# Kernel optimization log

Hardware: AMD Instinct MI355X
Metric: run time of the kernel (lower is better)

Reference implementation:

```python
import jax, jax.numpy as jnp
import numpy as np

B, S, D = 4, 4096, 2048
DH = D // 2
EPS = 1e-6


def setup_inputs() -> dict:
    key = jax.random.key(0)
    ks = jax.random.split(key, 6)
    return {
        "inputs": jax.random.normal(ks[0], (B * S, D), jnp.float32),
        "lf1_cache": jax.random.normal(ks[1], (B, D, 1, 1), jnp.float32),
        "lf2_cache": jax.random.normal(ks[2], (B, DH, 1, 1), jnp.float32),
        "w1": jax.random.normal(ks[3], (DH, D, 2), jnp.float32) / np.sqrt(2.0 * D).astype(np.float32),
        "b1": jnp.zeros((DH,), jnp.float32),
        "w2": jax.random.normal(ks[4], (D, DH, 2), jnp.float32) / np.sqrt(2.0 * DH).astype(np.float32),
        "b2": jnp.zeros((D,), jnp.float32),
        "ln_w": jnp.ones((D,), jnp.float32),
    }


def reference(inputs, lf1_cache, lf2_cache, w1, b1, w2, b2, ln_w):
    # inputs: [B*S, D] flat tokens; caches hold one previous timestep per batch.
    x = inputs.reshape(B, S, D)
    # prepend cached timestep -> [B, S+1, D]  (equiv. to torch.cat along conv time dim)
    x_cat = jnp.concatenate([lf1_cache[:, :, 0, 0][:, None, :], x], axis=1)
    # conv1: kernel size 2 over time, dense over channels (groups=1)
    # o1[b,t,e] = sum_d w1[e,d,0]*x_cat[b,t,d] + w1[e,d,1]*x_cat[b,t+1,d] + b1[e]
    o1 = (jnp.einsum('btd,ed->bte', x_cat[:, :-1], w1[:, :, 0])
          + jnp.einsum('btd,ed->bte', x_cat[:, 1:], w1[:, :, 1]) + b1)  # [B,S,DH]
    o1_cat = jnp.concatenate([lf2_cache[:, :, 0, 0][:, None, :], o1], axis=1)  # [B,S+1,DH]
    o2 = (jnp.einsum('bte,de->btd', o1_cat[:, :-1], w2[:, :, 0])
          + jnp.einsum('bte,de->btd', o1_cat[:, 1:], w2[:, :, 1]) + b2)  # [B,S,D]
    y = o2 + x  # residual add
    # RMSNorm over the channel dim
    inv_rms = jax.lax.rsqrt(jnp.mean(y * y, axis=-1, keepdims=True) + EPS)
    lf_output = y * inv_rms * ln_w  # [B, S, D]
    # new caches: last timestep of conv1 input and conv2 input, in [B,C,1,1] layout
    lf1 = x_cat[:, -1][:, :, None, None]
    lf2 = o1_cat[:, -1][:, :, None, None]
    return lf_output, lf1, lf2
```

## Files before the change

### kernel.cpp

```cpp
#include <hip/hip_runtime.h>
#include <cstdint>

#define BB 4
#define SS 4096
#define DD 2048
#define DH 1024
#define MM (BB * SS)
#define EPSV 1e-6f

typedef unsigned short u16;
typedef __bf16 bf16x8 __attribute__((ext_vector_type(8)));
typedef float f32x4 __attribute__((ext_vector_type(4)));


__device__ __forceinline__ u16 f2bf(float f) {
    uint32_t u = __float_as_uint(f);
    u += 0x7fffu + ((u >> 16) & 1u);
    return (u16)(u >> 16);
}

__device__ __forceinline__ void async16(const void* g, void* l) {
    __builtin_amdgcn_global_load_lds(
        (const __attribute__((address_space(1))) uint32_t*)g,
        (__attribute__((address_space(3))) uint32_t*)l,
        16, 0, 0);
}

#define FENCE asm volatile("" ::: "memory")


__global__ void cvt_f32_bf16(const float* __restrict__ in, u16* __restrict__ out, long n4) {
    long i = (long)blockIdx.x * blockDim.x + threadIdx.x;
    if (i >= n4) return;
    float4 v = *(const float4*)(in + i * 4);
    ushort4 o;
    o.x = f2bf(v.x); o.y = f2bf(v.y); o.z = f2bf(v.z); o.w = f2bf(v.w);
    *(ushort4*)(out + i * 4) = o;
}

__global__ void pack_w(const float* __restrict__ in, u16* __restrict__ out, int dshift) {
    int idx = blockIdx.x * 256 + threadIdx.x;
    int Dd = 1 << dshift;
    int e = idx >> dshift;
    int d = idx & (Dd - 1);
    float2 v = *(const float2*)(in + (long)idx * 2);
    long rowbase = (long)e * (Dd * 2);
    out[rowbase + d] = f2bf(v.x);
    out[rowbase + Dd + d] = f2bf(v.y);
}

template <int KD, int MODE>
__launch_bounds__(512, 2)
__global__ void gemm2tap(const u16* __restrict__ A,
                         const u16* __restrict__ cache,
                         const u16* __restrict__ Bt,
                         const float* __restrict__ bias,
                         u16* __restrict__ obf,
                         float* __restrict__ lf2out,
                         const float* __restrict__ xres,
                         float* __restrict__ yout)
{
    constexpr int KTOT = 2 * KD;
    constexpr int NT = KTOT / 64;
    constexpr int NS = 2 * NT;
    constexpr int NN = (MODE == 1) ? DH : DD;
    static_assert(NS % 4 == 0 && NS >= 8, "ring-4 schedule needs NS % 4 == 0, NS >= 8");

    const int tid = threadIdx.x;
    const int lane = tid & 63;
    const int wave = tid >> 6;
    const int bm = blockIdx.x;
    const int bn = blockIdx.y;

    __shared__ __align__(16) u16 sm[65536];

    const int srow = wave * 16 + (lane >> 2);
    const int skc  = (lane & 3) ^ ((lane >> 3) & 3);
    const int sRowA = wave * 512;

    const u16 *aPrev0, *aPrev1, *aCur0, *aCur1, *bPtr0, *bPtr1;
    {
        long r0 = (long)bm * 256 + srow;
        long r1 = r0 + 128;
        aCur0 = A + r0 * KD + skc * 8;
        aCur1 = A + r1 * KD + skc * 8;
        aPrev0 = ((((int)r0) & (SS - 1)) == 0) ? (cache + (r0 >> 12) * KD + skc * 8)
                                               : (A + (r0 - 1) * KD + skc * 8);
        aPrev1 = ((((int)r1) & (SS - 1)) == 0) ? (cache + (r1 >> 12) * KD + skc * 8)
                                               : (A + (r1 - 1) * KD + skc * 8);
        long n0l = (long)bn * 256 + srow;
        bPtr0 = Bt + n0l * KTOT + skc * 8;
        bPtr1 = Bt + (n0l + 128) * KTOT + skc * 8;
    }

#define STAGE(SLOT_, U_) do {                                                  \
        const int _u = (U_);                                                   \
        const u16 *_g0, *_g1;                                                  \
        if (_u < NT) { _g0 = aPrev0 + _u * 32; _g1 = aPrev1 + _u * 32; }       \
        else { _g0 = aCur0 + (_u - NT) * 32; _g1 = aCur1 + (_u - NT) * 32; }   \
        async16(_g0, sm + (SLOT_) * 8192 + sRowA);                             \
        async16(_g1, sm + (SLOT_) * 8192 + 4096 + sRowA);                      \
        async16(bPtr0 + _u * 32, sm + 32768 + (SLOT_) * 8192 + sRowA);         \
        async16(bPtr1 + _u * 32, sm + 32768 + (SLOT_) * 8192 + 4096 + sRowA);  \
    } while (0)

    const int frow = lane & 15;
    const int fquad = lane >> 4;
    const int wm128 = (wave >> 2) * 128;
    const int wn64  = (wave & 3) * 64;
    const int fq8s = (fquad ^ ((frow >> 1) & 3)) * 8;
    const int afb = (wm128 + frow) * 32 + fq8s;
    const int bfb = (wn64 + frow) * 32 + fq8s;

    f32x4 acc[8][4];
#pragma unroll
    for (int i = 0; i < 8; ++i)
#pragma unroll
        for (int j = 0; j < 4; ++j)
            acc[i][j] = (f32x4){0.f, 0.f, 0.f, 0.f};

#define MFMA_(D_, A_, B_) D_ = __builtin_amdgcn_mfma_f32_16x16x32_bf16(A_, B_, D_, 0, 0, 0)

#define STEP(SLOT_, U3_, DOSTG_, VMS_)                                         \
  {                                                                            \
    const u16* aro = sm + (SLOT_) * 8192;                                      \
    const u16* bro = sm + 32768 + (SLOT_) * 8192;                              \
    bf16x8 bq[4], af[8];                                                       \
    _Pragma("unroll")                                                          \
    for (int nf = 0; nf < 4; ++nf)                                             \
        bq[nf] = *(const bf16x8*)(bro + bfb + nf * 512);                       \
    _Pragma("unroll")                                                          \
    for (int mf = 0; mf < 8; ++mf)                                             \
        af[mf] = *(const bf16x8*)(aro + afb + mf * 512);                       \
    if (DOSTG_) STAGE((((SLOT_) + 3) & 3), (U3_));                             \
    __builtin_amdgcn_s_setprio(1);                                             \
    _Pragma("unroll")                                                          \
    for (int mf = 0; mf < 8; ++mf)                                             \
        _Pragma("unroll")                                                      \
        for (int nf = 0; nf < 4; ++nf)                                         \
            MFMA_(acc[mf][nf], af[mf], bq[nf]);                                \
    __builtin_amdgcn_s_setprio(0);                                             \
    asm volatile(VMS_ ::: "memory");                                           \
    FENCE; __builtin_amdgcn_s_barrier(); FENCE;                                \
  }

    STAGE(0, 0); FENCE;
    STAGE(1, 1); FENCE;
    STAGE(2, 2);
    asm volatile("s_waitcnt vmcnt(8)" ::: "memory");
    FENCE; __builtin_amdgcn_s_barrier(); FENCE;

    for (int s = 0; s < NS - 4; s += 4) {
        STEP(0, s + 3, 1, "s_waitcnt vmcnt(8)");
        STEP(1, s + 4, 1, "s_waitcnt vmcnt(8)");
        STEP(2, s + 5, 1, "s_waitcnt vmcnt(8)");
        STEP(3, s + 6, 1, "s_waitcnt vmcnt(8)");
    }
    STEP(0, NS - 1, 1, "s_waitcnt vmcnt(8)");
    STEP(1, 0, 0, "s_waitcnt vmcnt(4)");
    STEP(2, 0, 0, "s_waitcnt vmcnt(0)");
    STEP(3, 0, 0, "");

#undef STEP
#undef STAGE

    const long m0 = (long)bm * 256 + wm128;
    const int n0 = bn * 256 + wn64;
#pragma unroll
    for (int mf = 0; mf < 8; ++mf) {
#pragma unroll
        for (int nf = 0; nf < 4; ++nf) {
            const int n = n0 + nf * 16 + frow;
            const float bv = bias[n];
#pragma unroll
            for (int v = 0; v < 4; ++v) {
                const long m = m0 + mf * 16 + fquad * 4 + v;
                float val = acc[mf][nf][v] + bv;
                if (MODE == 1) {
                    obf[m * NN + n] = f2bf(val);
                    if ((((int)m) & (SS - 1)) == (SS - 1))
                        lf2out[(m >> 12) * NN + n] = val;
                } else {
                    val += xres[m * NN + n];
                    yout[m * NN + n] = val;
                }
            }
        }
    }
}


__global__ void rmsnorm_inplace(float* __restrict__ y, const float* __restrict__ lnw) {
    const long r = blockIdx.x;
    float* row = y + r * DD;
    const int tid = threadIdx.x;

    float4 v0 = *(float4*)(row + tid * 4);
    float4 v1 = *(float4*)(row + 1024 + tid * 4);
    float s = v0.x * v0.x + v0.y * v0.y + v0.z * v0.z + v0.w * v0.w
            + v1.x * v1.x + v1.y * v1.y + v1.z * v1.z + v1.w * v1.w;
#pragma unroll
    for (int off = 32; off; off >>= 1) s += __shfl_xor(s, off, 64);

    __shared__ float red[4];
    if ((tid & 63) == 0) red[tid >> 6] = s;
    __syncthreads();
    float tot = red[0] + red[1] + red[2] + red[3];
    float inv = rsqrtf(tot * (1.0f / DD) + EPSV);

    float4 w0 = *(const float4*)(lnw + tid * 4);
    float4 w1 = *(const float4*)(lnw + 1024 + tid * 4);
    v0.x *= inv * w0.x; v0.y *= inv * w0.y; v0.z *= inv * w0.z; v0.w *= inv * w0.w;
    v1.x *= inv * w1.x; v1.y *= inv * w1.y; v1.z *= inv * w1.z; v1.w *= inv * w1.w;
    *(float4*)(row + tid * 4) = v0;
    *(float4*)(row + 1024 + tid * 4) = v1;
}

__global__ void lf1_copy(const float* __restrict__ x, float* __restrict__ out) {
    int idx = blockIdx.x * 256 + threadIdx.x;
    int b = idx >> 11;
    int d = idx & (DD - 1);
    out[idx] = x[((long)b * SS + (SS - 1)) * DD + d];
}


extern "C" void kernel_launch(void* const* d_in, const int* in_sizes, int n_in,
                              void* d_out, int out_size, void* d_ws, size_t ws_size,
                              hipStream_t stream) {
    const float* x    = (const float*)d_in[0];
    const float* lf1c = (const float*)d_in[1];
    const float* lf2c = (const float*)d_in[2];
    const float* w1   = (const float*)d_in[3];
    const float* b1   = (const float*)d_in[4];
    const float* w2   = (const float*)d_in[5];
    const float* b2   = (const float*)d_in[6];
    const float* lnw  = (const float*)d_in[7];

    float* out    = (float*)d_out;
    float* lf1out = out + (long)MM * DD;
    float* lf2out = lf1out + (long)BB * DD;

    char* ws = (char*)d_ws;
    u16* Xbf  = (u16*)ws; ws += (long)MM * DD * 2;
    u16* o1bf = (u16*)ws; ws += (long)MM * DH * 2;
    u16* W1b  = (u16*)ws; ws += (long)DH * (2 * DD) * 2;
    u16* W2b  = (u16*)ws; ws += (long)DD * (2 * DH) * 2;
    u16* c1   = (u16*)ws; ws += (long)BB * DD * 2;
    u16* c2   = (u16*)ws; ws += (long)BB * DH * 2;

    cvt_f32_bf16<<<32768, 256, 0, stream>>>(x, Xbf, (long)MM * DD / 4);
    cvt_f32_bf16<<<8, 256, 0, stream>>>(lf1c, c1, (long)BB * DD / 4);
    cvt_f32_bf16<<<4, 256, 0, stream>>>(lf2c, c2, (long)BB * DH / 4);
    pack_w<<<(DH * DD) / 256, 256, 0, stream>>>(w1, W1b, 11);
    pack_w<<<(DD * DH) / 256, 256, 0, stream>>>(w2, W2b, 10);

    gemm2tap<DD, 1><<<dim3(MM / 256, DH / 256), 512, 0, stream>>>(
        Xbf, c1, W1b, b1, o1bf, lf2out, nullptr, nullptr);

    gemm2tap<DH, 2><<<dim3(MM / 256, DD / 256), 512, 0, stream>>>(
        o1bf, c2, W2b, b2, nullptr, nullptr, x, out);

    rmsnorm_inplace<<<MM, 256, 0, stream>>>(out, lnw);
    lf1_copy<<<BB * DD / 256, 256, 0, stream>>>(x, lf1out);
}
```

Before: 555.4 us.

## Double-buffer LDS fragment registers so MFMAs overlap next-slot LDS reads

Restructures the GEMM main loop so each window issues LDS reads for the next ring slot into a second register set while MFMAs consume the previous set (register ping-pong). Stage slot indices are now derived from the k-step, and vmcnt waits and barriers are retimed to match a one-step-ahead read schedule. The aim is to hide LDS read latency behind MFMA execution. The cost is doubling the fragment registers (24 more bf16x8 vectors), which at launch bounds 512x2 may cause spills or lower occupancy, and the tighter vmcnt/barrier pattern carries a risk of races on the 4-slot ring.

```diff
diff --git a/kernel.cpp b/kernel.cpp
--- a/kernel.cpp
+++ b/kernel.cpp
@@ -65,6 +65,7 @@
     constexpr int NS = 2 * NT;
     constexpr int NN = (MODE == 1) ? DH : DD;
     static_assert(NS % 4 == 0 && NS >= 8, "ring-4 schedule needs NS % 4 == 0, NS >= 8");
+    static_assert(((NS - 4) & 1) == 0, "A/B frag parity needs even main-loop window count");
 
     const int tid = threadIdx.x;
     const int lane = tid & 63;
@@ -93,15 +94,16 @@
         bPtr1 = Bt + (n0l + 128) * KTOT + skc * 8;
     }
 
-#define STAGE(SLOT_, U_) do {                                                  \
+#define STAGE(U_) do {                                                         \
         const int _u = (U_);                                                   \
+        const int _sl = _u & 3;                                                \
         const u16 *_g0, *_g1;                                                  \
         if (_u < NT) { _g0 = aPrev0 + _u * 32; _g1 = aPrev1 + _u * 32; }       \
         else { _g0 = aCur0 + (_u - NT) * 32; _g1 = aCur1 + (_u - NT) * 32; }   \
-        async16(_g0, sm + (SLOT_) * 8192 + sRowA);                             \
-        async16(_g1, sm + (SLOT_) * 8192 + 4096 + sRowA);                      \
-        async16(bPtr0 + _u * 32, sm + 32768 + (SLOT_) * 8192 + sRowA);         \
-        async16(bPtr1 + _u * 32, sm + 32768 + (SLOT_) * 8192 + 4096 + sRowA);  \
+        async16(_g0, sm + _sl * 8192 + sRowA);                                 \
+        async16(_g1, sm + _sl * 8192 + 4096 + sRowA);                          \
+        async16(bPtr0 + _u * 32, sm + 32768 + _sl * 8192 + sRowA);             \
+        async16(bPtr1 + _u * 32, sm + 32768 + _sl * 8192 + 4096 + sRowA);      \
     } while (0)
 
     const int frow = lane & 15;
@@ -119,49 +121,59 @@
         for (int j = 0; j < 4; ++j)
             acc[i][j] = (f32x4){0.f, 0.f, 0.f, 0.f};
 
-#define MFMA_(D_, A_, B_) D_ = __builtin_amdgcn_mfma_f32_16x16x32_bf16(A_, B_, D_, 0, 0, 0)
-
-#define STEP(SLOT_, U3_, DOSTG_, VMS_)                                         \
-  {                                                                            \
-    const u16* aro = sm + (SLOT_) * 8192;                                      \
-    const u16* bro = sm + 32768 + (SLOT_) * 8192;                              \
-    bf16x8 bq[4], af[8];                                                       \
+    bf16x8 afA[8], bqA[4], afB[8], bqB[4];
+
+#define READS(SET_, RSLOT_) do {                                               \
+    const u16* _aro = sm + (RSLOT_) * 8192;                                    \
+    const u16* _bro = sm + 32768 + (RSLOT_) * 8192;                            \
     _Pragma("unroll")                                                          \
     for (int nf = 0; nf < 4; ++nf)                                             \
-        bq[nf] = *(const bf16x8*)(bro + bfb + nf * 512);                       \
+        bq##SET_[nf] = *(const bf16x8*)(_bro + bfb + nf * 512);                \
     _Pragma("unroll")                                                          \
     for (int mf = 0; mf < 8; ++mf)                                             \
-        af[mf] = *(const bf16x8*)(aro + afb + mf * 512);                       \
-    if (DOSTG_) STAGE((((SLOT_) + 3) & 3), (U3_));                             \
+        af##SET_[mf] = *(const bf16x8*)(_aro + afb + mf * 512);                \
+} while (0)
+
+#define MFMA_(D_, A_, B_) D_ = __builtin_amdgcn_mfma_f32_16x16x32_bf16(A_, B_, D_, 0, 0, 0)
+
+#define MFMAS(SET_) do {                                                       \
     __builtin_amdgcn_s_setprio(1);                                             \
     _Pragma("unroll")                                                          \
     for (int mf = 0; mf < 8; ++mf)                                             \
         _Pragma("unroll")                                                      \
         for (int nf = 0; nf < 4; ++nf)                                         \
-            MFMA_(acc[mf][nf], af[mf], bq[nf]);                                \
+            MFMA_(acc[mf][nf], af##SET_[mf], bq##SET_[nf]);                    \
     __builtin_amdgcn_s_setprio(0);                                             \
+} while (0)
+
+#define WIN(RSLOT_, RSET_, MSET_, SU_, DOSTG_, VMS_, DOBAR_)                   \
+  {                                                                            \
+    READS(RSET_, (RSLOT_));                                                    \
+    if (DOSTG_) STAGE((SU_));                                                  \
+    MFMAS(MSET_);                                                              \
     asm volatile(VMS_ ::: "memory");                                           \
-    FENCE; __builtin_amdgcn_s_barrier(); FENCE;                                \
+    if (DOBAR_) { __builtin_amdgcn_s_barrier(); FENCE; }                       \
   }
 
-    STAGE(0, 0); FENCE;
-    STAGE(1, 1); FENCE;
-    STAGE(2, 2);
-    asm volatile("s_waitcnt vmcnt(8)" ::: "memory");
+    STAGE(0); FENCE;
+    STAGE(1); FENCE;
+    STAGE(2);
+    asm volatile("s_waitcnt vmcnt(4)" ::: "memory");
     FENCE; __builtin_amdgcn_s_barrier(); FENCE;
-
-    for (int s = 0; s < NS - 4; s += 4) {
-        STEP(0, s + 3, 1, "s_waitcnt vmcnt(8)");
-        STEP(1, s + 4, 1, "s_waitcnt vmcnt(8)");
-        STEP(2, s + 5, 1, "s_waitcnt vmcnt(8)");
-        STEP(3, s + 6, 1, "s_waitcnt vmcnt(8)");
+    READS(A, 0);
+
+    for (int s = 0; s < NS - 4; s += 2) {
+        WIN((s + 1) & 3, B, A, s + 3, 1, "s_waitcnt vmcnt(4)", 1);
+        WIN((s + 2) & 3, A, B, s + 4, 1, "s_waitcnt vmcnt(4)", 1);
     }
-    STEP(0, NS - 1, 1, "s_waitcnt vmcnt(8)");
-    STEP(1, 0, 0, "s_waitcnt vmcnt(4)");
-    STEP(2, 0, 0, "s_waitcnt vmcnt(0)");
-    STEP(3, 0, 0, "");
-
-#undef STEP
+    WIN((NS - 3) & 3, B, A, NS - 1, 1, "s_waitcnt vmcnt(4)", 1);
+    WIN((NS - 2) & 3, A, B, 0, 0, "s_waitcnt vmcnt(0)", 1);
+    WIN((NS - 1) & 3, B, A, 0, 0, "", 0);
+    MFMAS(B);
+
+#undef WIN
+#undef MFMAS
+#undef READS
 #undef STAGE
 
     const long m0 = (long)bm * 256 + wm128;
```

Result: no change. 564.2 us (+1.6%).
